# Performance work log

Measured on AMD Instinct MI355X. Metric: run time of the kernel, lower is better.

## Reference

```python
import jax, jax.numpy as jnp
import numpy as np

N_HEADS = 16
ROPE_THETA = 10000.0


def _rope(x):
    # x: (b, h, t, d). Interleaved-pair rotary embedding (lucidrains
    # rotary_embedding_torch convention: rotate_half on (d r) pairs, r=2).
    b, h, t, d = x.shape
    inv_freq = 1.0 / (ROPE_THETA ** (jnp.arange(0, d, 2, dtype=jnp.float32) / d))  # (d/2,)
    ang = jnp.arange(t, dtype=jnp.float32)[:, None] * inv_freq[None, :]            # (t, d/2)
    cos = jnp.cos(ang)
    sin = jnp.sin(ang)
    xp = x.reshape(b, h, t, d // 2, 2)
    x1, x2 = xp[..., 0], xp[..., 1]
    o1 = x1 * cos - x2 * sin
    o2 = x1 * sin + x2 * cos
    return jnp.stack([o1, o2], axis=-1).reshape(b, h, t, d)


def setup_inputs() -> dict:
    key = jax.random.key(0)
    k1, k2, k3 = jax.random.split(key, 3)
    B, T, C = 4, 2048, 1024
    x = jax.random.normal(k1, (B, T, C), dtype=jnp.float32)
    # torch nn.Linear weight layout: (out_features, in_features)
    w_attn = jax.random.normal(k2, (3 * C, C), dtype=jnp.float32) * (1.0 / np.sqrt(C))
    w_proj = jax.random.normal(k3, (C, C), dtype=jnp.float32) * (1.0 / np.sqrt(C))
    return {"x": x, "w_attn": w_attn, "w_proj": w_proj}


def reference(x, w_attn, w_proj):
    B, T, C = x.shape
    H = N_HEADS
    D = C // H
    # fused QKV projection: (b, t, 3C)
    qkv = jnp.einsum('btc,fc->btf', x, w_attn)
    # rearrange 'b t (r h d) -> r b h t d'
    qkv = qkv.reshape(B, T, 3, H, D).transpose(2, 0, 3, 1, 4)
    q, k, v = qkv[0], qkv[1], qkv[2]
    q = _rope(q)
    k = _rope(k)
    scale = 1.0 / np.sqrt(D).astype(np.float32)
    scores = jnp.einsum('bhqd,bhkd->bhqk', q, k) * scale
    attn = jax.nn.softmax(scores, axis=-1)
    y = jnp.einsum('bhqk,bhkd->bhqd', attn, v)       # (b, h, t, d)
    y = y.transpose(0, 2, 1, 3).reshape(B, T, C)     # 'b h t d -> b t (h d)'
    return jnp.einsum('btc,oc->bto', y, w_proj)
```

## Files before the change

### kernel.cpp

```cpp
#include <hip/hip_runtime.h>
#include <hip/hip_bf16.h>
#include <math.h>

typedef __bf16 bf16;
typedef float f32x4 __attribute__((ext_vector_type(4)));
typedef float f32x16 __attribute__((ext_vector_type(16)));
typedef bf16 bf16x8 __attribute__((ext_vector_type(8)));
typedef bf16 bf16x4 __attribute__((ext_vector_type(4)));
typedef unsigned int uint;

#define MFMA16(a, b, c) __builtin_amdgcn_mfma_f32_16x16x32_bf16(a, b, c, 0, 0, 0)
#define MFMA32(a, b, c) __builtin_amdgcn_mfma_f32_32x32x16_bf16(a, b, c, 0, 0, 0)

static constexpr int T_SEQ = 2048;
static constexpr int CDIM  = 1024;
static constexpr int NH    = 16;
static constexpr int DH    = 64;
static constexpr float FREQ_C = 0.20762050593045998f;

__device__ __forceinline__ void gld_lds16(const bf16* g, bf16* l) {
    __builtin_amdgcn_global_load_lds(
        (const __attribute__((address_space(1))) void*)g,
        (__attribute__((address_space(3))) void*)l, 16, 0, 0);
}

__device__ __forceinline__ void fast_sincos(float x, float* s, float* c) {
    const float INV2PI = 0.15915494309189535f;
    const float PI2_HI = 6.28125f;
    const float PI2_LO = 1.9353071795864769e-3f;
    const float n = rintf(x * INV2PI);
    float r = fmaf(-n, PI2_HI, x);
    r = fmaf(-n, PI2_LO, r);
    *s = __sinf(r);
    *c = __cosf(r);
}

__global__ __launch_bounds__(256)
void rope_table(float2* __restrict__ tab) {
    const int i = blockIdx.x * 256 + threadIdx.x;
    const int t = i >> 5, p = i & 31;
    const float ang = (float)t * exp2f(-2.0f * (float)p * FREQ_C);
    float s, c;
    fast_sincos(ang, &s, &c);
    tab[i] = make_float2(c, s);
}

__global__ __launch_bounds__(256)
void cvt_f32_bf16(const float* __restrict__ in, bf16* __restrict__ out, int n8) {
    const int i = blockIdx.x * 256 + threadIdx.x;
    if (i >= n8) return;
    const f32x4* p = (const f32x4*)(in + (size_t)i * 8);
    const f32x4 lo = p[0], hi = p[1];
    bf16x8 o;
    o[0] = (bf16)lo[0]; o[1] = (bf16)lo[1]; o[2] = (bf16)lo[2]; o[3] = (bf16)lo[3];
    o[4] = (bf16)hi[0]; o[5] = (bf16)hi[1]; o[6] = (bf16)hi[2]; o[7] = (bf16)hi[3];
    *(bf16x8*)(out + (size_t)i * 8) = o;
}

#define GEMM_CORE(Abase, Bbase, KDIM)                                            \
    f32x4 acc[4][4] = {};                                                        \
    for (int kk = 0; kk < (KDIM); kk += 64) {                                    \
        __syncthreads();                                                         \
        _Pragma("unroll")                                                        \
        for (int u = 0; u < 4; u++) {                                            \
            const int st = wave * 4 + u, mg = st >> 1, kg = st & 1;              \
            gld_lds16(Abase + (size_t)(mg * 16 + sm) * (KDIM) + kk + kg * 32 + sc * 8, \
                      &ash[st * 512]);                                           \
            gld_lds16(Bbase + (size_t)(mg * 16 + sm) * (KDIM) + kk + kg * 32 + sc * 8, \
                      &bsh[st * 512]);                                           \
        }                                                                        \
        __syncthreads();                                                         \
        _Pragma("unroll")                                                        \
        for (int kg = 0; kg < 2; kg++) {                                         \
            bf16x8 af[4], bfr[4];                                                \
            _Pragma("unroll")                                                    \
            for (int a = 0; a < 4; a++)                                          \
                af[a] = *(const bf16x8*)&ash[((wm * 4 + a) * 2 + kg) * 512 + lane * 8]; \
            _Pragma("unroll")                                                    \
            for (int b = 0; b < 4; b++)                                          \
                bfr[b] = *(const bf16x8*)&bsh[((wn * 4 + b) * 2 + kg) * 512 + lane * 8]; \
            _Pragma("unroll")                                                    \
            for (int a = 0; a < 4; a++)                                          \
                _Pragma("unroll")                                                \
                for (int b = 0; b < 4; b++)                                      \
                    acc[a][b] = MFMA16(af[a], bfr[b], acc[a][b]);                \
        }                                                                        \
    }

__global__ __launch_bounds__(256)
void gemm_qkv(const bf16* __restrict__ X, const bf16* __restrict__ W,
              bf16* __restrict__ Qo, bf16* __restrict__ Ko, bf16* __restrict__ Vt,
              const float2* __restrict__ tab) {
    __shared__ __align__(16) bf16 ash[16 * 512];
    __shared__ __align__(16) bf16 bsh[16 * 512];
    const int tid = threadIdx.x, lane = tid & 63, wave = tid >> 6;
    const int quad = lane >> 4, l16 = lane & 15;
    const int wm = wave >> 1, wn = wave & 1;
    const int bm = blockIdx.y, bn = blockIdx.x;
    const int sm = lane & 15, sc = lane >> 4;

    const bf16* Abase = X + (size_t)(bm * 128) * CDIM;
    const bf16* Bbase = W + (size_t)(bn * 128) * CDIM;
    GEMM_CORE(Abase, Bbase, CDIM)

    const int rr    = (bn * 128) >> 10;
    const int nsec  = (bn * 128) & 1023;
    const int batch = (bm * 128) >> 11;
    const int tb    = ((bm * 128) & 2047) + wm * 64;

    if (rr == 2) {
#pragma unroll
        for (int b = 0; b < 4; b++) {
            const int n = nsec + wn * 64 + b * 16 + l16;
            const int h = n >> 6, d = n & 63;
            bf16* vp = Vt + ((size_t)(batch * NH + h) * DH + d) * T_SEQ;
#pragma unroll
            for (int a = 0; a < 4; a++) {
                const int t0 = tb + a * 16 + quad * 4;
                bf16x4 pk4 = { (bf16)acc[a][b][0], (bf16)acc[a][b][1],
                               (bf16)acc[a][b][2], (bf16)acc[a][b][3] };
                *(bf16x4*)(vp + t0) = pk4;
            }
        }
    } else {
        bf16* Dst = (rr == 0) ? Qo : Ko;
        const float scale = (rr == 0) ? 0.125f : 1.0f;
#pragma unroll
        for (int b = 0; b < 4; b++) {
            const int n = nsec + wn * 64 + b * 16 + l16;
            const int h = n >> 6, d = n & 63;
            const int p = d >> 1, odd = d & 1;
            bf16* dp = Dst + (size_t)(batch * NH + h) * T_SEQ * DH + d;
#pragma unroll
            for (int a = 0; a < 4; a++) {
#pragma unroll
                for (int r = 0; r < 4; r++) {
                    const int t = tb + a * 16 + quad * 4 + r;
                    const float val = acc[a][b][r];
                    const float partner = __shfl_xor(val, 1);
                    const float2 cs = tab[t * 32 + p];
                    float o = odd ? (partner * cs.y + val * cs.x)
                                  : (val * cs.x - partner * cs.y);
                    dp[(size_t)t * DH] = (bf16)(o * scale);
                }
            }
        }
    }
}

__global__ __launch_bounds__(256)
void gemm_proj(const bf16* __restrict__ X, const bf16* __restrict__ W,
               float* __restrict__ Out) {
    __shared__ __align__(16) bf16 ash[16 * 512];
    __shared__ __align__(16) bf16 bsh[16 * 512];
    const int tid = threadIdx.x, lane = tid & 63, wave = tid >> 6;
    const int quad = lane >> 4, l16 = lane & 15;
    const int wm = wave >> 1, wn = wave & 1;
    const int bm = blockIdx.y, bn = blockIdx.x;
    const int sm = lane & 15, sc = lane >> 4;

    const bf16* Abase = X + (size_t)(bm * 128) * CDIM;
    const bf16* Bbase = W + (size_t)(bn * 128) * CDIM;
    GEMM_CORE(Abase, Bbase, CDIM)

#pragma unroll
    for (int b = 0; b < 4; b++) {
        const int n = bn * 128 + wn * 64 + b * 16 + l16;
#pragma unroll
        for (int a = 0; a < 4; a++) {
            const int m = bm * 128 + wm * 64 + a * 16 + quad * 4;
#pragma unroll
            for (int r = 0; r < 4; r++)
                Out[(size_t)(m + r) * CDIM + n] = acc[a][b][r];
        }
    }
}

__global__ __launch_bounds__(256)
void flash(const bf16* __restrict__ Q, const bf16* __restrict__ K,
           const bf16* __restrict__ Vt, bf16* __restrict__ Y) {
    __shared__ __align__(16) bf16 ksh[8 * 512];
    __shared__ __align__(16) bf16 vsh[8 * 512];
    const int tid = threadIdx.x, lane = tid & 63, wave = tid >> 6;
    const int l32 = lane & 31, hi = lane >> 5;
    const int id = blockIdx.x;
    const int bh = (id & 7) * 8 + ((id >> 3) & 7);
    const int qb = id >> 6;
    const size_t kbase = (size_t)bh * T_SEQ * DH;
    const size_t vbase = (size_t)bh * DH * T_SEQ;
    const int q0 = qb * 128 + wave * 32;

    bf16x8 bq[4];
    const bf16* qp = Q + kbase + (size_t)(q0 + l32) * DH + hi * 8;
#pragma unroll
    for (int c = 0; c < 4; c++) bq[c] = *(const bf16x8*)(qp + c * 16);

    f32x16 oT[2] = {};
    float li = 0.f;

    for (int kt = 0; kt < T_SEQ; kt += 64) {
        __syncthreads();
        if (wave < 2) {
#pragma unroll
            for (int u = 0; u < 4; u++) {
                const int s = wave * 4 + u, kb = s >> 2, c = s & 3;
                gld_lds16(K + kbase + (size_t)(kt + kb * 32 + l32) * DH
                              + c * 16 + hi * 8,
                          &ksh[s * 512]);
            }
        } else {
#pragma unroll
            for (int u = 0; u < 4; u++) {
                const int s = (wave - 2) * 4 + u, db = s >> 2, kc = s & 3;
                gld_lds16(Vt + vbase + (size_t)(db * 32 + l32) * T_SEQ
                              + kt + kc * 16 + hi * 8,
                          &vsh[s * 512]);
            }
        }
        __syncthreads();

#pragma unroll
        for (int kb = 0; kb < 2; kb++) {
            f32x16 s = {};
#pragma unroll
            for (int c = 0; c < 4; c++) {
                const bf16x8 a = *(const bf16x8*)&ksh[(kb * 4 + c) * 512 + lane * 8];
                s = MFMA32(a, bq[c], s);
            }
            uint P[8], S8[8];
#pragma unroll
            for (int w = 0; w < 8; w++) {
                const float e0 = __expf(s[2 * w]);
                const float e1 = __expf(s[2 * w + 1]);
                li += e0 + e1;
                union { __hip_bfloat162 v; uint u; } cv;
                cv.v = __float22bfloat162_rn(make_float2(e0, e1));
                P[w] = cv.u;
            }
#pragma unroll
            for (int w = 0; w < 8; w++)
                S8[w] = (uint)__shfl_xor((int)P[w], 32);
#pragma unroll
            for (int t = 0; t < 2; t++) {
                union { uint u[4]; bf16x8 v; } bP;
                bP.u[0] = hi ? S8[4 * t + 2] : P[4 * t + 0];
                bP.u[1] = hi ? S8[4 * t + 3] : P[4 * t + 1];
                bP.u[2] = hi ? P[4 * t + 2] : S8[4 * t + 0];
                bP.u[3] = hi ? P[4 * t + 3] : S8[4 * t + 1];
                const int kc = kb * 2 + t;
#pragma unroll
                for (int db = 0; db < 2; db++) {
                    const bf16x8 a = *(const bf16x8*)&vsh[(db * 4 + kc) * 512 + lane * 8];
                    oT[db] = MFMA32(a, bP.v, oT[db]);
                }
            }
        }
    }

    li += __shfl_xor(li, 32);
    const float inv = 1.0f / li;

    const int b = bh >> 4, h = bh & 15;
    const size_t yrow = ((size_t)b * T_SEQ + q0 + l32) * CDIM + h * DH;
#pragma unroll
    for (int db = 0; db < 2; db++)
#pragma unroll
        for (int rg = 0; rg < 4; rg++) {
            bf16x4 o4 = { (bf16)(oT[db][rg * 4 + 0] * inv),
                          (bf16)(oT[db][rg * 4 + 1] * inv),
                          (bf16)(oT[db][rg * 4 + 2] * inv),
                          (bf16)(oT[db][rg * 4 + 3] * inv) };
            *(bf16x4*)(Y + yrow + db * 32 + 8 * rg + 4 * hi) = o4;
        }
}

extern "C" void kernel_launch(void* const* d_in, const int* in_sizes, int n_in,
                              void* d_out, int out_size, void* d_ws, size_t ws_size,
                              hipStream_t stream) {
    const float* x      = (const float*)d_in[0];
    const float* w_attn = (const float*)d_in[1];
    const float* w_proj = (const float*)d_in[2];
    float* out = (float*)d_out;

    bf16* ws = (bf16*)d_ws;
    const size_t SZ = (size_t)4 * NH * T_SEQ * DH;
    bf16* Xb  = ws;
    bf16* Wab = Xb + SZ;
    bf16* Wpb = Wab + 3145728;
    bf16* Qb  = Wpb + 1048576;
    bf16* Kb  = Qb + SZ;
    bf16* Vtb = Kb + SZ;
    bf16* Yb  = Vtb + SZ;
    float2* tab = (float2*)(Yb + SZ);

    rope_table<<<256, 256, 0, stream>>>(tab);
    cvt_f32_bf16<<<4096, 256, 0, stream>>>(x, Xb, 1048576);
    cvt_f32_bf16<<<1536, 256, 0, stream>>>(w_attn, Wab, 393216);
    cvt_f32_bf16<<<512, 256, 0, stream>>>(w_proj, Wpb, 131072);

    gemm_qkv<<<dim3(24, 64), 256, 0, stream>>>(Xb, Wab, Qb, Kb, Vtb, tab);
    flash<<<1024, 256, 0, stream>>>(Qb, Kb, Vtb, Yb);
    gemm_proj<<<dim3(8, 64), 256, 0, stream>>>(Yb, Wpb, out);
}
```

Measured before the change: 360.9 us.

## Double-buffer K/V tiles in flash attention and use exp2 with folded log2e

The flash attention kernel now keeps two LDS buffers for the K and V tiles. It issues the asynchronous global-to-LDS loads for the next 64-key tile while computing on the current one, which also drops one barrier per iteration. This is meant to hide global load latency behind MFMA and softmax work, at the cost of doubling LDS use per block, which may reduce occupancy. Separately, log2(e) is folded into the Q pre-scale so the softmax can use exp2f instead of __expf, removing a multiply per score.

```diff
diff --git a/kernel.cpp b/kernel.cpp
--- a/kernel.cpp
+++ b/kernel.cpp
@@ -17,6 +17,7 @@
 static constexpr int NH    = 16;
 static constexpr int DH    = 64;
 static constexpr float FREQ_C = 0.20762050593045998f;
+static constexpr float Q_SCALE = 0.18033688011112042f;
 
 __device__ __forceinline__ void gld_lds16(const bf16* g, bf16* l) {
     __builtin_amdgcn_global_load_lds(
@@ -124,7 +125,7 @@
         }
     } else {
         bf16* Dst = (rr == 0) ? Qo : Ko;
-        const float scale = (rr == 0) ? 0.125f : 1.0f;
+        const float scale = (rr == 0) ? Q_SCALE : 1.0f;
 #pragma unroll
         for (int b = 0; b < 4; b++) {
             const int n = nsec + wn * 64 + b * 16 + l16;
@@ -179,8 +180,8 @@
 __global__ __launch_bounds__(256)
 void flash(const bf16* __restrict__ Q, const bf16* __restrict__ K,
            const bf16* __restrict__ Vt, bf16* __restrict__ Y) {
-    __shared__ __align__(16) bf16 ksh[8 * 512];
-    __shared__ __align__(16) bf16 vsh[8 * 512];
+    __shared__ __align__(16) bf16 ksh[2][8 * 512];
+    __shared__ __align__(16) bf16 vsh[2][8 * 512];
     const int tid = threadIdx.x, lane = tid & 63, wave = tid >> 6;
     const int l32 = lane & 31, hi = lane >> 5;
     const int id = blockIdx.x;
@@ -198,40 +199,45 @@
     f32x16 oT[2] = {};
     float li = 0.f;
 
-    for (int kt = 0; kt < T_SEQ; kt += 64) {
+#define STAGE(buf_, kt_) do {                                              \
+        if (wave < 2) {                                                    \
+            _Pragma("unroll")                                              \
+            for (int u = 0; u < 4; u++) {                                  \
+                const int s = wave * 4 + u, kb = s >> 2, c = s & 3;        \
+                gld_lds16(K + kbase + (size_t)((kt_) + kb * 32 + l32) * DH \
+                              + c * 16 + hi * 8,                           \
+                          &ksh[buf_][s * 512]);                            \
+            }                                                              \
+        } else {                                                           \
+            _Pragma("unroll")                                              \
+            for (int u = 0; u < 4; u++) {                                  \
+                const int s = (wave - 2) * 4 + u, db = s >> 2, kc = s & 3; \
+                gld_lds16(Vt + vbase + (size_t)(db * 32 + l32) * T_SEQ     \
+                              + (kt_) + kc * 16 + hi * 8,                  \
+                          &vsh[buf_][s * 512]);                            \
+            }                                                              \
+        }                                                                  \
+    } while (0)
+
+    STAGE(0, 0);
+    int ib = 0;
+    for (int kt = 0; kt < T_SEQ; kt += 64, ib ^= 1) {
         __syncthreads();
-        if (wave < 2) {
-#pragma unroll
-            for (int u = 0; u < 4; u++) {
-                const int s = wave * 4 + u, kb = s >> 2, c = s & 3;
-                gld_lds16(K + kbase + (size_t)(kt + kb * 32 + l32) * DH
-                              + c * 16 + hi * 8,
-                          &ksh[s * 512]);
-            }
-        } else {
-#pragma unroll
-            for (int u = 0; u < 4; u++) {
-                const int s = (wave - 2) * 4 + u, db = s >> 2, kc = s & 3;
-                gld_lds16(Vt + vbase + (size_t)(db * 32 + l32) * T_SEQ
-                              + kt + kc * 16 + hi * 8,
-                          &vsh[s * 512]);
-            }
-        }
-        __syncthreads();
+        if (kt + 64 < T_SEQ) STAGE(ib ^ 1, kt + 64);
 
 #pragma unroll
         for (int kb = 0; kb < 2; kb++) {
             f32x16 s = {};
 #pragma unroll
             for (int c = 0; c < 4; c++) {
-                const bf16x8 a = *(const bf16x8*)&ksh[(kb * 4 + c) * 512 + lane * 8];
+                const bf16x8 a = *(const bf16x8*)&ksh[ib][(kb * 4 + c) * 512 + lane * 8];
                 s = MFMA32(a, bq[c], s);
             }
             uint P[8], S8[8];
 #pragma unroll
             for (int w = 0; w < 8; w++) {
-                const float e0 = __expf(s[2 * w]);
-                const float e1 = __expf(s[2 * w + 1]);
+                const float e0 = exp2f(s[2 * w]);
+                const float e1 = exp2f(s[2 * w + 1]);
                 li += e0 + e1;
                 union { __hip_bfloat162 v; uint u; } cv;
                 cv.v = __float22bfloat162_rn(make_float2(e0, e1));
@@ -250,12 +256,13 @@
                 const int kc = kb * 2 + t;
 #pragma unroll
                 for (int db = 0; db < 2; db++) {
-                    const bf16x8 a = *(const bf16x8*)&vsh[(db * 4 + kc) * 512 + lane * 8];
+                    const bf16x8 a = *(const bf16x8*)&vsh[ib][(db * 4 + kc) * 512 + lane * 8];
                     oT[db] = MFMA32(a, bP.v, oT[db]);
                 }
             }
         }
     }
+#undef STAGE
 
     li += __shfl_xor(li, 32);
     const float inv = 1.0f / li;
```

Measured after the change: 358.8 us. Within noise of the previous version (-0.6%).
